# Optimization experiments

Measured on AMD Instinct MI355X. Metric: run time of the kernel, lower is better.

Reference implementation:

```python
import jax, jax.numpy as jnp
import numpy as np

N = 50000      # nodes
E = 1600000    # directed edges (avg degree 32)
IN_DIM = 64
OUT_DIM = 64


def setup_inputs() -> dict:
    key = jax.random.key(0)
    ks = jax.random.split(key, 8)
    mu = jax.random.normal(ks[0], (N, IN_DIM), dtype=jnp.float32)
    x = jax.random.normal(ks[1], (N, 1), dtype=jnp.float32)
    edge_index = jax.random.randint(ks[2], (2, E), 0, N, dtype=jnp.int64)
    edge_w = jax.random.uniform(ks[3], (E,), dtype=jnp.float32)
    # torch nn.Linear(in, out, bias=False) weight has shape [out, in]
    W1 = jax.random.normal(ks[4], (OUT_DIM, 1), dtype=jnp.float32) * (1.0 / 1.0)
    W2 = jax.random.normal(ks[5], (OUT_DIM, 1), dtype=jnp.float32) * (1.0 / 1.0)
    W3 = jax.random.normal(ks[6], (OUT_DIM, IN_DIM), dtype=jnp.float32) * (1.0 / np.sqrt(IN_DIM))
    W4 = jax.random.normal(ks[7], (OUT_DIM, 3 * OUT_DIM), dtype=jnp.float32) * (1.0 / np.sqrt(3 * OUT_DIM))
    return {"mu": mu, "x": x, "edge_index": edge_index, "edge_w": edge_w,
            "W1": W1, "W2": W2, "W3": W3, "W4": W4}


def reference(mu, x, edge_index, edge_w, W1, W2, W3, W4):
    relu = jax.nn.relu
    n_nodes = mu.shape[0]
    # per-node / per-edge embeddings
    h_x = relu(x @ W1.T)                       # [N, out]
    h_e = relu(edge_w[:, None] @ W2.T)         # [E, out]
    h_mu = relu(mu @ W3.T)                     # [N, out]
    dst = edge_index[1]                        # gather side (reverse-direction message passing)
    src = edge_index[0]                        # scatter side
    # gather, concat along feature dim -> [E, 3*out]
    cat_feat = jnp.concatenate([h_x[dst], h_e, h_mu[dst]], axis=1)
    # scatter_add over destination row 0 -> [N, 3*out]
    agg = jax.ops.segment_sum(cat_feat, src, num_segments=n_nodes)
    agg = relu(agg @ W4.T)                     # [N, out]
    return relu(h_x + h_mu + agg)
```

## Files before the change

### kernel.cpp

```cpp
#include <hip/hip_runtime.h>


#define KBINS 512
#define BCHUNK 4096
#define CAPB 4096
#define CAPL 3500
#define MAXW 98

typedef __attribute__((ext_vector_type(8))) short short8;
typedef __attribute__((ext_vector_type(4))) float f32x4;
typedef __attribute__((ext_vector_type(4))) unsigned short u16x4;

__device__ inline unsigned short to_bf16(float f) {
    unsigned u = __float_as_uint(f);
    return (unsigned short)((u + 0x7FFFu + ((u >> 16) & 1u)) >> 16);
}

__global__ void k_prep(const float* __restrict__ W1, const float* __restrict__ W2,
                       const float* __restrict__ W3, const float* __restrict__ W4,
                       short* __restrict__ gB1, short* __restrict__ gB2,
                       float* __restrict__ gvec, unsigned* __restrict__ gcursor) {
    __shared__ float sa[64], sb[64];
    int t = threadIdx.x;
    gcursor[t] = 0u;
    gcursor[256 + t] = 0u;
    if (t < 64) {
        float w1 = W1[t];
        sa[t] = fmaxf(w1, 0.f);
        sb[t] = fmaxf(-w1, 0.f);
        gvec[t] = sa[t];
        gvec[64 + t] = sb[t];
    }
    __syncthreads();
    if (t < 64) {
        float s1 = 0.f, s2 = 0.f, s3 = 0.f;
#pragma unroll 8
        for (int o = 0; o < 64; ++o) {
            float w4a = W4[t * 192 + o];
            float w4b = W4[t * 192 + 64 + o];
            s1 += w4a * sa[o];
            s2 += w4a * sb[o];
            s3 += w4b * fmaxf(W2[o], 0.f);
        }
        gvec[128 + t] = s1;
        gvec[192 + t] = s2;
        gvec[256 + t] = s3;
    }
    for (int idx = t; idx < 4096; idx += 256) {
        int j = idx >> 6, k = idx & 63;
        int lane = ((k >> 3) & 3) * 16 + (j & 15);
        int pos = (((j >> 4) * 2 + (k >> 5)) * 64 + lane) * 8 + (k & 7);
        gB1[pos] = (short)to_bf16(W3[idx]);
        gB2[pos] = (short)to_bf16(W4[j * 192 + 128 + k]);
    }
}

__global__ void __launch_bounds__(512, 8) k_hb(
    const float* __restrict__ mu, const float* __restrict__ x,
    const short* __restrict__ gB1, const short* __restrict__ gB2,
    const float* __restrict__ gvec,
    unsigned short* __restrict__ base, unsigned short* __restrict__ hc2,
    const int* __restrict__ ei, const float* __restrict__ ew,
    unsigned* __restrict__ gcursor, unsigned* __restrict__ bins,
    int N, int E) {
    __shared__ __align__(16) char smem[35840];
    short* sB1 = (short*)smem;
    short* sB2 = (short*)(smem + 8192);
    float* sAv = (float*)(smem + 16384);
    float* sBv = (float*)(smem + 16640);
    float* sVA = (float*)(smem + 16896);
    float* sVB = (float*)(smem + 17152);
    short* sA  = (short*)(smem + 17408);
    unsigned* cnt   = (unsigned*)smem;
    unsigned* basel = (unsigned*)(smem + 2048);
    unsigned* gbase = (unsigned*)(smem + 4096);
    unsigned* wsum  = (unsigned*)(smem + 6144);
    unsigned* wpre  = (unsigned*)(smem + 6176);
    unsigned* stage = (unsigned*)(smem + 6208);
    unsigned short* binof = (unsigned short*)(smem + 22592);

    int t = threadIdx.x;
    int wave = t >> 6, l = t & 63;

    for (int i = t; i < 512; i += 512) {
        ((short8*)sB1)[i] = ((const short8*)gB1)[i];
        ((short8*)sB2)[i] = ((const short8*)gB2)[i];
    }
    if (t >= 512 - 256) {
        int v = t - (512 - 256);
        if (v < 64) sAv[v] = gvec[v];
        else if (v < 128) sBv[v - 64] = gvec[64 + (v - 64)];
        else if (v < 192) sVA[v - 128] = gvec[128 + (v - 128)];
        else sVB[v - 192] = gvec[192 + (v - 192)];
    }
    __syncthreads();

    int n0 = (blockIdx.x * 8 + wave) * 16;
    if (n0 < N) {
        short* A1 = sA + wave * 2304 / 2;
        {
            int srow = l >> 2, scol = (l & 3) * 16;
            bool rok = (n0 + srow) < N;
            const float4* gp = (const float4*)(mu + (size_t)(n0 + srow) * 64 + scol);
            float4 m0 = {}, m1 = {}, m2 = {}, m3 = {};
            if (rok) { m0 = gp[0]; m1 = gp[1]; m2 = gp[2]; m3 = gp[3]; }
            short8 v0, v1;
            v0[0]=to_bf16(m0.x); v0[1]=to_bf16(m0.y); v0[2]=to_bf16(m0.z); v0[3]=to_bf16(m0.w);
            v0[4]=to_bf16(m1.x); v0[5]=to_bf16(m1.y); v0[6]=to_bf16(m1.z); v0[7]=to_bf16(m1.w);
            v1[0]=to_bf16(m2.x); v1[1]=to_bf16(m2.y); v1[2]=to_bf16(m2.z); v1[3]=to_bf16(m2.w);
            v1[4]=to_bf16(m3.x); v1[5]=to_bf16(m3.y); v1[6]=to_bf16(m3.z); v1[7]=to_bf16(m3.w);
            *(short8*)&A1[srow * 72 + scol] = v0;
            *(short8*)&A1[srow * 72 + scol + 8] = v1;
        }
        float pr[4], qr[4];
#pragma unroll
        for (int r = 0; r < 4; ++r) {
            int nr = n0 + (l >> 4) * 4 + r;
            float xv = (nr < N) ? x[nr] : 0.f;
            pr[r] = fmaxf(xv, 0.f);
            qr[r] = fmaxf(-xv, 0.f);
        }
        f32x4 acc[4] = {};
        {
            short8 a0 = *(const short8*)&A1[(l & 15) * 72 + ((l >> 4) * 8)];
            short8 a1 = *(const short8*)&A1[(l & 15) * 72 + 32 + ((l >> 4) * 8)];
#pragma unroll
            for (int jt = 0; jt < 4; ++jt) {
                short8 b0 = *(const short8*)&sB1[((jt * 2 + 0) * 64 + l) * 8];
                short8 b1 = *(const short8*)&sB1[((jt * 2 + 1) * 64 + l) * 8];
                acc[jt] = __builtin_amdgcn_mfma_f32_16x16x32_bf16(a0, b0, acc[jt], 0, 0, 0);
                acc[jt] = __builtin_amdgcn_mfma_f32_16x16x32_bf16(a1, b1, acc[jt], 0, 0, 0);
            }
        }
#pragma unroll
        for (int jt = 0; jt < 4; ++jt) {
            int jc = jt * 16 + (l & 15);
            float aj = sAv[jc], bj = sBv[jc];
#pragma unroll
            for (int r = 0; r < 4; ++r) {
                int row = (l >> 4) * 4 + r;
                float h = fmaxf(acc[jt][r], 0.f);
                A1[row * 72 + jc] = (short)to_bf16(h);
                int nr = n0 + row;
                if (nr < N) base[(size_t)nr * 64 + jc] = to_bf16(pr[r] * aj + qr[r] * bj + h);
            }
        }
        f32x4 acc2[4] = {};
        {
            short8 a0 = *(const short8*)&A1[(l & 15) * 72 + ((l >> 4) * 8)];
            short8 a1 = *(const short8*)&A1[(l & 15) * 72 + 32 + ((l >> 4) * 8)];
#pragma unroll
            for (int jt = 0; jt < 4; ++jt) {
                short8 b0 = *(const short8*)&sB2[((jt * 2 + 0) * 64 + l) * 8];
                short8 b1 = *(const short8*)&sB2[((jt * 2 + 1) * 64 + l) * 8];
                acc2[jt] = __builtin_amdgcn_mfma_f32_16x16x32_bf16(a0, b0, acc2[jt], 0, 0, 0);
                acc2[jt] = __builtin_amdgcn_mfma_f32_16x16x32_bf16(a1, b1, acc2[jt], 0, 0, 0);
            }
        }
#pragma unroll
        for (int jt = 0; jt < 4; ++jt) {
            int jc = jt * 16 + (l & 15);
            float vaj = sVA[jc], vbj = sVB[jc];
#pragma unroll
            for (int r = 0; r < 4; ++r) {
                int nr = n0 + (l >> 4) * 4 + r;
                if (nr < N)
                    hc2[(size_t)nr * 64 + jc] =
                        to_bf16(acc2[jt][r] + pr[r] * vaj + qr[r] * vbj);
            }
        }
    }
    __syncthreads();

    for (int c0 = blockIdx.x * BCHUNK; c0 < E; c0 += gridDim.x * BCHUNK) {
        cnt[t] = 0;
        __syncthreads();
        int mybin[8]; unsigned myrank[8]; unsigned myrec[8]; bool ok[8];
#pragma unroll
        for (int k = 0; k < 8; ++k) {
            int e = c0 + t + k * 512;
            ok[k] = (e < E);
            if (ok[k]) {
                int s = ei[e];
                int d = ei[E + e];
                unsigned wq = (unsigned)(ew[e] * 512.0f + 0.5f);
                if (wq > 511u) wq = 511u;
                unsigned b = ((unsigned)s * (unsigned)KBINS) / (unsigned)N;
                unsigned start = ((unsigned)b * (unsigned)N + KBINS - 1) / KBINS;
                unsigned sl = (unsigned)s - start;
                myrec[k] = (unsigned)d | (sl << 16) | (wq << 23);
                mybin[k] = (int)b;
                myrank[k] = atomicAdd(&cnt[b], 1u);
            }
        }
        __syncthreads();
        {
            unsigned v = cnt[t];
            unsigned sc = v;
#pragma unroll
            for (int off = 1; off < 64; off <<= 1) {
                unsigned u = (unsigned)__shfl_up((int)sc, off, 64);
                if (l >= off) sc += u;
            }
            if (l == 63) wsum[wave] = sc;
            __syncthreads();
            if (t < 8) {
                unsigned s = 0;
                for (int i = 0; i < t; ++i) s += wsum[i];
                wpre[t] = s;
            }
            __syncthreads();
            unsigned excl = sc - v + wpre[wave];
            basel[t] = excl;
            if (v) gbase[t] = atomicAdd(&gcursor[t], v);
        }
        __syncthreads();
#pragma unroll
        for (int k = 0; k < 8; ++k) if (ok[k]) {
            unsigned pos = basel[mybin[k]] + myrank[k];
            stage[pos] = myrec[k];
            binof[pos] = (unsigned short)mybin[k];
        }
        __syncthreads();
        int total = E - c0; if (total > BCHUNK) total = BCHUNK;
#pragma unroll
        for (int k = 0; k < 8; ++k) {
            int i = t + k * 512;
            if (i < total) {
                int b = binof[i];
                unsigned dst = gbase[b] + (unsigned)i - basel[b];
                if (dst < CAPB) bins[(size_t)b * CAPB + dst] = stage[i];
            }
        }
        __syncthreads();
    }
}

__global__ void __launch_bounds__(1024) k_agg(
    const unsigned short* __restrict__ hc2, const unsigned short* __restrict__ base,
    const unsigned* __restrict__ gcursor, const unsigned* __restrict__ bins,
    const float* __restrict__ gvec, float* __restrict__ out, int N) {
    __shared__ unsigned srec[CAPL];
    __shared__ unsigned hist[128];
    __shared__ unsigned sbase[128];
    __shared__ __align__(16) float svs[64];
    int b = blockIdx.x;
    int t = threadIdx.x;
    if (t < 128) hist[t] = 0;
    if (t >= 128 && t < 192) svs[t - 128] = gvec[256 + (t - 128)];
    int start = (b * N + KBINS - 1) / KBINS;
    int endn  = ((b + 1) * N + KBINS - 1) / KBINS;
    if (endn > N) endn = N;
    int W = endn - start;
    if (W > MAXW) W = MAXW;
    __syncthreads();
    int cntb = (int)gcursor[b];
    if (cntb > CAPB) cntb = CAPB;
    const unsigned* rec = bins + (size_t)b * CAPB;
    unsigned r[4]; unsigned rank[4]; bool ok[4];
#pragma unroll
    for (int k = 0; k < 4; ++k) {
        int i = t + k * 1024;
        ok[k] = (i < cntb);
        if (ok[k]) {
            r[k] = rec[i];
            rank[k] = atomicAdd(&hist[(r[k] >> 16) & 0x7Fu], 1u);
        }
    }
    __syncthreads();
    if (t < 64) {
        unsigned h0 = hist[2 * t], h1 = hist[2 * t + 1];
        unsigned s = h0 + h1;
#pragma unroll
        for (int off = 1; off < 64; off <<= 1) {
            unsigned u = (unsigned)__shfl_up((int)s, off, 64);
            if (t >= off) s += u;
        }
        sbase[2 * t]     = s - h1 - h0;
        sbase[2 * t + 1] = s - h1;
    }
    __syncthreads();
#pragma unroll
    for (int k = 0; k < 4; ++k) if (ok[k]) {
        unsigned pos = sbase[(r[k] >> 16) & 0x7Fu] + rank[k];
        if (pos < CAPL) srec[pos] = r[k];
    }
    __syncthreads();
    int wave = t >> 6, l = t & 63;
    int g = l >> 4, m = l & 15;
    f32x4 vsv = *(const f32x4*)&svs[m * 4];
    const float sc512 = 1.0f / 512.0f;
    for (int sl = wave; sl < W; sl += 16) {
        int beg = (int)sbase[sl];
        int end = beg + (int)hist[sl];
        if (beg > CAPL) beg = CAPL;
        if (end > CAPL) end = CAPL;
        f32x4 acc = {0.f, 0.f, 0.f, 0.f};
        float swn = 0.f;
        int i = beg;
        for (; i + 16 <= end; i += 16) {
            unsigned r0 = srec[i + g];
            unsigned r1 = srec[i + 4 + g];
            unsigned r2 = srec[i + 8 + g];
            unsigned r3 = srec[i + 12 + g];
            u16x4 u0 = *(const u16x4*)(hc2 + (size_t)(r0 & 0xFFFFu) * 64 + m * 4);
            u16x4 u1 = *(const u16x4*)(hc2 + (size_t)(r1 & 0xFFFFu) * 64 + m * 4);
            u16x4 u2 = *(const u16x4*)(hc2 + (size_t)(r2 & 0xFFFFu) * 64 + m * 4);
            u16x4 u3 = *(const u16x4*)(hc2 + (size_t)(r3 & 0xFFFFu) * 64 + m * 4);
#pragma unroll
            for (int k = 0; k < 4; ++k) {
                acc[k] += __uint_as_float((unsigned)u0[k] << 16)
                        + __uint_as_float((unsigned)u1[k] << 16)
                        + __uint_as_float((unsigned)u2[k] << 16)
                        + __uint_as_float((unsigned)u3[k] << 16);
            }
            swn += (float)(r0 >> 23) + (float)(r1 >> 23)
                 + (float)(r2 >> 23) + (float)(r3 >> 23);
        }
        for (; i + 8 <= end; i += 8) {
            unsigned r0 = srec[i + g];
            unsigned r1 = srec[i + 4 + g];
            u16x4 u0 = *(const u16x4*)(hc2 + (size_t)(r0 & 0xFFFFu) * 64 + m * 4);
            u16x4 u1 = *(const u16x4*)(hc2 + (size_t)(r1 & 0xFFFFu) * 64 + m * 4);
#pragma unroll
            for (int k = 0; k < 4; ++k) {
                acc[k] += __uint_as_float((unsigned)u0[k] << 16)
                        + __uint_as_float((unsigned)u1[k] << 16);
            }
            swn += (float)(r0 >> 23) + (float)(r1 >> 23);
        }
        for (; i < end; i += 4) {
            if (i + g < end) {
                unsigned r0 = srec[i + g];
                u16x4 u0 = *(const u16x4*)(hc2 + (size_t)(r0 & 0xFFFFu) * 64 + m * 4);
#pragma unroll
                for (int k = 0; k < 4; ++k)
                    acc[k] += __uint_as_float((unsigned)u0[k] << 16);
                swn += (float)(r0 >> 23);
            }
        }
#pragma unroll
        for (int off = 16; off < 64; off <<= 1) {
            acc[0] += __shfl_xor(acc[0], off, 64);
            acc[1] += __shfl_xor(acc[1], off, 64);
            acc[2] += __shfl_xor(acc[2], off, 64);
            acc[3] += __shfl_xor(acc[3], off, 64);
            swn    += __shfl_xor(swn, off, 64);
        }
        if (g == 0) {
            size_t gi = (size_t)(start + sl) * 64 + m * 4;
            u16x4 bv = *(const u16x4*)(base + gi);
            f32x4 o;
#pragma unroll
            for (int k = 0; k < 4; ++k) {
                float aggv = fmaxf(swn * (vsv[k] * sc512) + acc[k], 0.f);
                float bval = __uint_as_float(((unsigned)bv[k]) << 16);
                o[k] = fmaxf(bval + aggv, 0.f);
            }
            *(f32x4*)&out[gi] = o;
        }
    }
}

extern "C" void kernel_launch(void* const* d_in, const int* in_sizes, int n_in,
                              void* d_out, int out_size, void* d_ws, size_t ws_size,
                              hipStream_t stream) {
    const float* mu = (const float*)d_in[0];
    const float* x  = (const float*)d_in[1];
    const int*   ei = (const int*)d_in[2];
    const float* ew = (const float*)d_in[3];
    const float* W1 = (const float*)d_in[4];
    const float* W2 = (const float*)d_in[5];
    const float* W3 = (const float*)d_in[6];
    const float* W4 = (const float*)d_in[7];
    float* out = (float*)d_out;

    const int N = in_sizes[1];
    const int E = in_sizes[3];

    unsigned short* base = (unsigned short*)d_ws;
    unsigned short* hc2 = base + (size_t)N * 64;
    unsigned* bins = (unsigned*)(hc2 + (size_t)N * 64);
    unsigned* gcursor = bins + (size_t)KBINS * CAPB;
    short* gB1 = (short*)(gcursor + KBINS);
    short* gB2 = gB1 + 4096;
    float* gvec = (float*)(gB2 + 4096);

    k_prep<<<1, 256, 0, stream>>>(W1, W2, W3, W4, gB1, gB2, gvec, gcursor);

    int hblocks = (N + 127) / 128;
    int chunks = (E + BCHUNK - 1) / BCHUNK;
    int grid = hblocks > chunks ? hblocks : chunks;
    k_hb<<<grid, 512, 0, stream>>>(mu, x, gB1, gB2, gvec, base, hc2,
                                   ei, ew, gcursor, bins, N, E);

    k_agg<<<KBINS, 1024, 0, stream>>>(hc2, base, gcursor, bins, gvec, out, N);
}
```

Before: 57.46 us.

## Sub-bucket edges by source-row range and rotate gather order per XCC

Edge records in each aggregation block are now bucketed by a combined key: the local slot plus the top two bits of the gathered node index. This gives 512 histogram buckets, built with a two-level wave prefix scan. Each wave then walks its slot's four sub-buckets in an order rotated by the hardware XCC id, read via s_getreg. The aim is to spread concurrent gathers across XCDs over different quarters of the hc2 table for better L2 locality. The cost is a larger shared histogram, an extra scan stage and synchronisation, and the loss of the 16-wide unrolled gather loop.

```diff
diff --git a/kernel.cpp b/kernel.cpp
--- a/kernel.cpp
+++ b/kernel.cpp
@@ -6,6 +6,7 @@
 #define CAPB 4096
 #define CAPL 3500
 #define MAXW 98
+#define XCC_IMM (20 | (31 << 11))
 
 typedef __attribute__((ext_vector_type(8))) short short8;
 typedef __attribute__((ext_vector_type(4))) float f32x4;
@@ -241,13 +242,15 @@
     const unsigned* __restrict__ gcursor, const unsigned* __restrict__ bins,
     const float* __restrict__ gvec, float* __restrict__ out, int N) {
     __shared__ unsigned srec[CAPL];
-    __shared__ unsigned hist[128];
-    __shared__ unsigned sbase[128];
+    __shared__ unsigned hist[512];
+    __shared__ unsigned sbase[512];
+    __shared__ unsigned wsum[8], wpre[8];
     __shared__ __align__(16) float svs[64];
     int b = blockIdx.x;
     int t = threadIdx.x;
-    if (t < 128) hist[t] = 0;
-    if (t >= 128 && t < 192) svs[t - 128] = gvec[256 + (t - 128)];
+    int wave = t >> 6, l = t & 63;
+    if (t < 512) hist[t] = 0;
+    if (t >= 512 && t < 576) svs[t - 512] = gvec[256 + (t - 512)];
     int start = (b * N + KBINS - 1) / KBINS;
     int endn  = ((b + 1) * N + KBINS - 1) / KBINS;
     if (endn > N) endn = N;
@@ -257,86 +260,81 @@
     int cntb = (int)gcursor[b];
     if (cntb > CAPB) cntb = CAPB;
     const unsigned* rec = bins + (size_t)b * CAPB;
-    unsigned r[4]; unsigned rank[4]; bool ok[4];
+    unsigned r[4]; unsigned rank[4]; unsigned key[4]; bool ok[4];
 #pragma unroll
     for (int k = 0; k < 4; ++k) {
         int i = t + k * 1024;
         ok[k] = (i < cntb);
         if (ok[k]) {
             r[k] = rec[i];
-            rank[k] = atomicAdd(&hist[(r[k] >> 16) & 0x7Fu], 1u);
-        }
-    }
-    __syncthreads();
-    if (t < 64) {
-        unsigned h0 = hist[2 * t], h1 = hist[2 * t + 1];
-        unsigned s = h0 + h1;
+            key[k] = (((r[k] & 0xFFFFu) >> 14) << 7) | ((r[k] >> 16) & 0x7Fu);
+            rank[k] = atomicAdd(&hist[key[k]], 1u);
+        }
+    }
+    __syncthreads();
+    unsigned scv = 0, vv = 0;
+    if (t < 512) {
+        vv = hist[t];
+        scv = vv;
 #pragma unroll
         for (int off = 1; off < 64; off <<= 1) {
-            unsigned u = (unsigned)__shfl_up((int)s, off, 64);
-            if (t >= off) s += u;
-        }
-        sbase[2 * t]     = s - h1 - h0;
-        sbase[2 * t + 1] = s - h1;
-    }
+            unsigned u = (unsigned)__shfl_up((int)scv, off, 64);
+            if (l >= off) scv += u;
+        }
+        if (l == 63) wsum[wave] = scv;
+    }
+    __syncthreads();
+    if (t < 8) {
+        unsigned s = 0;
+        for (int i = 0; i < t; ++i) s += wsum[i];
+        wpre[t] = s;
+    }
+    __syncthreads();
+    if (t < 512) sbase[t] = scv - vv + wpre[wave];
     __syncthreads();
 #pragma unroll
     for (int k = 0; k < 4; ++k) if (ok[k]) {
-        unsigned pos = sbase[(r[k] >> 16) & 0x7Fu] + rank[k];
+        unsigned pos = sbase[key[k]] + rank[k];
         if (pos < CAPL) srec[pos] = r[k];
     }
     __syncthreads();
-    int wave = t >> 6, l = t & 63;
     int g = l >> 4, m = l & 15;
     f32x4 vsv = *(const f32x4*)&svs[m * 4];
     const float sc512 = 1.0f / 512.0f;
+    unsigned rot = __builtin_amdgcn_s_getreg(XCC_IMM) & 3u;
     for (int sl = wave; sl < W; sl += 16) {
-        int beg = (int)sbase[sl];
-        int end = beg + (int)hist[sl];
-        if (beg > CAPL) beg = CAPL;
-        if (end > CAPL) end = CAPL;
         f32x4 acc = {0.f, 0.f, 0.f, 0.f};
         float swn = 0.f;
-        int i = beg;
-        for (; i + 16 <= end; i += 16) {
-            unsigned r0 = srec[i + g];
-            unsigned r1 = srec[i + 4 + g];
-            unsigned r2 = srec[i + 8 + g];
-            unsigned r3 = srec[i + 12 + g];
-            u16x4 u0 = *(const u16x4*)(hc2 + (size_t)(r0 & 0xFFFFu) * 64 + m * 4);
-            u16x4 u1 = *(const u16x4*)(hc2 + (size_t)(r1 & 0xFFFFu) * 64 + m * 4);
-            u16x4 u2 = *(const u16x4*)(hc2 + (size_t)(r2 & 0xFFFFu) * 64 + m * 4);
-            u16x4 u3 = *(const u16x4*)(hc2 + (size_t)(r3 & 0xFFFFu) * 64 + m * 4);
-#pragma unroll
-            for (int k = 0; k < 4; ++k) {
-                acc[k] += __uint_as_float((unsigned)u0[k] << 16)
-                        + __uint_as_float((unsigned)u1[k] << 16)
-                        + __uint_as_float((unsigned)u2[k] << 16)
-                        + __uint_as_float((unsigned)u3[k] << 16);
-            }
-            swn += (float)(r0 >> 23) + (float)(r1 >> 23)
-                 + (float)(r2 >> 23) + (float)(r3 >> 23);
-        }
-        for (; i + 8 <= end; i += 8) {
-            unsigned r0 = srec[i + g];
-            unsigned r1 = srec[i + 4 + g];
-            u16x4 u0 = *(const u16x4*)(hc2 + (size_t)(r0 & 0xFFFFu) * 64 + m * 4);
-            u16x4 u1 = *(const u16x4*)(hc2 + (size_t)(r1 & 0xFFFFu) * 64 + m * 4);
-#pragma unroll
-            for (int k = 0; k < 4; ++k) {
-                acc[k] += __uint_as_float((unsigned)u0[k] << 16)
-                        + __uint_as_float((unsigned)u1[k] << 16);
-            }
-            swn += (float)(r0 >> 23) + (float)(r1 >> 23);
-        }
-        for (; i < end; i += 4) {
-            if (i + g < end) {
+#pragma unroll
+        for (int s4 = 0; s4 < 4; ++s4) {
+            int sh = (s4 + (int)rot) & 3;
+            int kk = (sh << 7) | sl;
+            int beg = (int)sbase[kk];
+            int end = beg + (int)hist[kk];
+            if (beg > CAPL) beg = CAPL;
+            if (end > CAPL) end = CAPL;
+            int i = beg;
+            for (; i + 8 <= end; i += 8) {
                 unsigned r0 = srec[i + g];
+                unsigned r1 = srec[i + 4 + g];
                 u16x4 u0 = *(const u16x4*)(hc2 + (size_t)(r0 & 0xFFFFu) * 64 + m * 4);
-#pragma unroll
-                for (int k = 0; k < 4; ++k)
-                    acc[k] += __uint_as_float((unsigned)u0[k] << 16);
-                swn += (float)(r0 >> 23);
+                u16x4 u1 = *(const u16x4*)(hc2 + (size_t)(r1 & 0xFFFFu) * 64 + m * 4);
+#pragma unroll
+                for (int k = 0; k < 4; ++k) {
+                    acc[k] += __uint_as_float((unsigned)u0[k] << 16)
+                            + __uint_as_float((unsigned)u1[k] << 16);
+                }
+                swn += (float)(r0 >> 23) + (float)(r1 >> 23);
+            }
+            for (; i < end; i += 4) {
+                if (i + g < end) {
+                    unsigned r0 = srec[i + g];
+                    u16x4 u0 = *(const u16x4*)(hc2 + (size_t)(r0 & 0xFFFFu) * 64 + m * 4);
+#pragma unroll
+                    for (int k = 0; k < 4; ++k)
+                        acc[k] += __uint_as_float((unsigned)u0[k] << 16);
+                    swn += (float)(r0 >> 23);
+                }
             }
         }
 #pragma unroll
```

Measured after the change: 66.91 us. 1.16x slower.

## Fold weight-prep kernel into consumer kernels and vectorize edge loads

Applied to the files above, without the earlier changes.

Removes the single-block k_prep launch. Each k_hb block now computes the W1-derived vectors and the bf16 swizzled W3/W4 tiles straight into shared memory, and each k_agg block computes the W2·W4 vector itself, with the cursor reset handled by a hipMemsetAsync. The edge binning loop also switches to int4/float4 loads of 8 contiguous edges per thread instead of strided scalar loads. The goal is to drop one serialized tiny kernel and widen global loads, at the cost of redundant per-block weight computation and a changed edge-to-thread mapping.

```diff
diff --git a/kernel.cpp b/kernel.cpp
--- a/kernel.cpp
+++ b/kernel.cpp
@@ -16,49 +16,10 @@
     return (unsigned short)((u + 0x7FFFu + ((u >> 16) & 1u)) >> 16);
 }
 
-__global__ void k_prep(const float* __restrict__ W1, const float* __restrict__ W2,
-                       const float* __restrict__ W3, const float* __restrict__ W4,
-                       short* __restrict__ gB1, short* __restrict__ gB2,
-                       float* __restrict__ gvec, unsigned* __restrict__ gcursor) {
-    __shared__ float sa[64], sb[64];
-    int t = threadIdx.x;
-    gcursor[t] = 0u;
-    gcursor[256 + t] = 0u;
-    if (t < 64) {
-        float w1 = W1[t];
-        sa[t] = fmaxf(w1, 0.f);
-        sb[t] = fmaxf(-w1, 0.f);
-        gvec[t] = sa[t];
-        gvec[64 + t] = sb[t];
-    }
-    __syncthreads();
-    if (t < 64) {
-        float s1 = 0.f, s2 = 0.f, s3 = 0.f;
-#pragma unroll 8
-        for (int o = 0; o < 64; ++o) {
-            float w4a = W4[t * 192 + o];
-            float w4b = W4[t * 192 + 64 + o];
-            s1 += w4a * sa[o];
-            s2 += w4a * sb[o];
-            s3 += w4b * fmaxf(W2[o], 0.f);
-        }
-        gvec[128 + t] = s1;
-        gvec[192 + t] = s2;
-        gvec[256 + t] = s3;
-    }
-    for (int idx = t; idx < 4096; idx += 256) {
-        int j = idx >> 6, k = idx & 63;
-        int lane = ((k >> 3) & 3) * 16 + (j & 15);
-        int pos = (((j >> 4) * 2 + (k >> 5)) * 64 + lane) * 8 + (k & 7);
-        gB1[pos] = (short)to_bf16(W3[idx]);
-        gB2[pos] = (short)to_bf16(W4[j * 192 + 128 + k]);
-    }
-}
-
 __global__ void __launch_bounds__(512, 8) k_hb(
     const float* __restrict__ mu, const float* __restrict__ x,
-    const short* __restrict__ gB1, const short* __restrict__ gB2,
-    const float* __restrict__ gvec,
+    const float* __restrict__ W1, const float* __restrict__ W3,
+    const float* __restrict__ W4,
     unsigned short* __restrict__ base, unsigned short* __restrict__ hc2,
     const int* __restrict__ ei, const float* __restrict__ ew,
     unsigned* __restrict__ gcursor, unsigned* __restrict__ bins,
@@ -82,16 +43,27 @@
     int t = threadIdx.x;
     int wave = t >> 6, l = t & 63;
 
-    for (int i = t; i < 512; i += 512) {
-        ((short8*)sB1)[i] = ((const short8*)gB1)[i];
-        ((short8*)sB2)[i] = ((const short8*)gB2)[i];
-    }
-    if (t >= 512 - 256) {
-        int v = t - (512 - 256);
-        if (v < 64) sAv[v] = gvec[v];
-        else if (v < 128) sBv[v - 64] = gvec[64 + (v - 64)];
-        else if (v < 192) sVA[v - 128] = gvec[128 + (v - 128)];
-        else sVB[v - 192] = gvec[192 + (v - 192)];
+    if (t < 64) {
+        float w1 = W1[t];
+        sAv[t] = fmaxf(w1, 0.f);
+        sBv[t] = fmaxf(-w1, 0.f);
+        float s1 = 0.f, s2 = 0.f;
+#pragma unroll 8
+        for (int o = 0; o < 64; ++o) {
+            float wo = __shfl(w1, o, 64);
+            float w4a = W4[t * 192 + o];
+            s1 += w4a * fmaxf(wo, 0.f);
+            s2 += w4a * fmaxf(-wo, 0.f);
+        }
+        sVA[t] = s1;
+        sVB[t] = s2;
+    }
+    for (int idx = t; idx < 4096; idx += 512) {
+        int j = idx >> 6, k = idx & 63;
+        int lane = ((k >> 3) & 3) * 16 + (j & 15);
+        int pos = (((j >> 4) * 2 + (k >> 5)) * 64 + lane) * 8 + (k & 7);
+        sB1[pos] = (short)to_bf16(W3[idx]);
+        sB2[pos] = (short)to_bf16(W4[j * 192 + 128 + k]);
     }
     __syncthreads();
 
@@ -176,14 +148,39 @@
         cnt[t] = 0;
         __syncthreads();
         int mybin[8]; unsigned myrank[8]; unsigned myrec[8]; bool ok[8];
+        int ss[8]; int dd[8]; float ww[8];
+        int e0 = c0 + t * 8;
+        if (e0 + 8 <= E) {
+            int4 sa0 = ((const int4*)(ei + c0))[t * 2];
+            int4 sa1 = ((const int4*)(ei + c0))[t * 2 + 1];
+            int4 da0 = ((const int4*)(ei + E + c0))[t * 2];
+            int4 da1 = ((const int4*)(ei + E + c0))[t * 2 + 1];
+            float4 w0 = ((const float4*)(ew + c0))[t * 2];
+            float4 w1v = ((const float4*)(ew + c0))[t * 2 + 1];
+            ss[0]=sa0.x; ss[1]=sa0.y; ss[2]=sa0.z; ss[3]=sa0.w;
+            ss[4]=sa1.x; ss[5]=sa1.y; ss[6]=sa1.z; ss[7]=sa1.w;
+            dd[0]=da0.x; dd[1]=da0.y; dd[2]=da0.z; dd[3]=da0.w;
+            dd[4]=da1.x; dd[5]=da1.y; dd[6]=da1.z; dd[7]=da1.w;
+            ww[0]=w0.x; ww[1]=w0.y; ww[2]=w0.z; ww[3]=w0.w;
+            ww[4]=w1v.x; ww[5]=w1v.y; ww[6]=w1v.z; ww[7]=w1v.w;
+#pragma unroll
+            for (int k = 0; k < 8; ++k) ok[k] = true;
+        } else {
+#pragma unroll
+            for (int k = 0; k < 8; ++k) {
+                int e = e0 + k;
+                ok[k] = (e < E);
+                ss[k] = ok[k] ? ei[e] : 0;
+                dd[k] = ok[k] ? ei[E + e] : 0;
+                ww[k] = ok[k] ? ew[e] : 0.f;
+            }
+        }
 #pragma unroll
         for (int k = 0; k < 8; ++k) {
-            int e = c0 + t + k * 512;
-            ok[k] = (e < E);
             if (ok[k]) {
-                int s = ei[e];
-                int d = ei[E + e];
-                unsigned wq = (unsigned)(ew[e] * 512.0f + 0.5f);
+                int s = ss[k];
+                int d = dd[k];
+                unsigned wq = (unsigned)(ww[k] * 512.0f + 0.5f);
                 if (wq > 511u) wq = 511u;
                 unsigned b = ((unsigned)s * (unsigned)KBINS) / (unsigned)N;
                 unsigned start = ((unsigned)b * (unsigned)N + KBINS - 1) / KBINS;
@@ -239,7 +236,8 @@
 __global__ void __launch_bounds__(1024) k_agg(
     const unsigned short* __restrict__ hc2, const unsigned short* __restrict__ base,
     const unsigned* __restrict__ gcursor, const unsigned* __restrict__ bins,
-    const float* __restrict__ gvec, float* __restrict__ out, int N) {
+    const float* __restrict__ W2, const float* __restrict__ W4,
+    float* __restrict__ out, int N) {
     __shared__ unsigned srec[CAPL];
     __shared__ unsigned hist[128];
     __shared__ unsigned sbase[128];
@@ -247,7 +245,14 @@
     int b = blockIdx.x;
     int t = threadIdx.x;
     if (t < 128) hist[t] = 0;
-    if (t >= 128 && t < 192) svs[t - 128] = gvec[256 + (t - 128)];
+    if (t >= 128 && t < 192) {
+        int j = t - 128;
+        float s3 = 0.f;
+#pragma unroll 8
+        for (int o = 0; o < 64; ++o)
+            s3 += fmaxf(W2[o], 0.f) * W4[j * 192 + 64 + o];
+        svs[j] = s3;
+    }
     int start = (b * N + KBINS - 1) / KBINS;
     int endn  = ((b + 1) * N + KBINS - 1) / KBINS;
     if (endn > N) endn = N;
@@ -382,17 +387,14 @@
     unsigned short* hc2 = base + (size_t)N * 64;
     unsigned* bins = (unsigned*)(hc2 + (size_t)N * 64);
     unsigned* gcursor = bins + (size_t)KBINS * CAPB;
-    short* gB1 = (short*)(gcursor + KBINS);
-    short* gB2 = gB1 + 4096;
-    float* gvec = (float*)(gB2 + 4096);
-
-    k_prep<<<1, 256, 0, stream>>>(W1, W2, W3, W4, gB1, gB2, gvec, gcursor);
+
+    hipMemsetAsync(gcursor, 0, KBINS * sizeof(unsigned), stream);
 
     int hblocks = (N + 127) / 128;
     int chunks = (E + BCHUNK - 1) / BCHUNK;
     int grid = hblocks > chunks ? hblocks : chunks;
-    k_hb<<<grid, 512, 0, stream>>>(mu, x, gB1, gB2, gvec, base, hc2,
+    k_hb<<<grid, 512, 0, stream>>>(mu, x, W1, W3, W4, base, hc2,
                                    ei, ew, gcursor, bins, N, E);
 
-    k_agg<<<KBINS, 1024, 0, stream>>>(hc2, base, gcursor, bins, gvec, out, N);
+    k_agg<<<KBINS, 1024, 0, stream>>>(hc2, base, gcursor, bins, W2, W4, out, N);
 }
```

Result: slower. 62.86 us (+9.4%).
